# Kernel optimization log

Measured on AMD Instinct MI355X. Metric: run time of the kernel, lower is better.

## Reference

```python
import jax, jax.numpy as jnp
import numpy as np

EPROJS = 512
ODIM = 1024
DLAYERS = 2
DUNITS = 512
EMBED_DIM = 512
JOINT_DIM = 512
BLANK = 0
B, TMAX, LMAX = 4, 256, 63


def setup_inputs() -> dict:
    key = jax.random.key(0)
    ks = jax.random.split(key, 20)
    s = 0.05
    embed = jax.random.normal(ks[0], (ODIM, EMBED_DIM), jnp.float32) * s
    embed = embed.at[BLANK].set(0.0)  # padding_idx=blank
    inp = {
        "hs_pad": jax.random.normal(ks[1], (B, TMAX, EPROJS), jnp.float32),
        "hlens": jnp.full((B,), TMAX, jnp.int32),
        "ys_pad": jax.random.randint(ks[2], (B, LMAX), 0, ODIM, jnp.int64),
        "embed": embed,
        "W_ih0": jax.random.normal(ks[3], (4 * DUNITS, EMBED_DIM), jnp.float32) * s,
        "W_hh0": jax.random.normal(ks[4], (4 * DUNITS, DUNITS), jnp.float32) * s,
        "b_ih0": jax.random.normal(ks[5], (4 * DUNITS,), jnp.float32) * s,
        "b_hh0": jax.random.normal(ks[6], (4 * DUNITS,), jnp.float32) * s,
        "W_ih1": jax.random.normal(ks[7], (4 * DUNITS, DUNITS), jnp.float32) * s,
        "W_hh1": jax.random.normal(ks[8], (4 * DUNITS, DUNITS), jnp.float32) * s,
        "b_ih1": jax.random.normal(ks[9], (4 * DUNITS,), jnp.float32) * s,
        "b_hh1": jax.random.normal(ks[10], (4 * DUNITS,), jnp.float32) * s,
        "W_enc": jax.random.normal(ks[11], (JOINT_DIM, EPROJS), jnp.float32) * s,
        "b_enc": jax.random.normal(ks[12], (JOINT_DIM,), jnp.float32) * s,
        "W_dec": jax.random.normal(ks[13], (JOINT_DIM, DUNITS), jnp.float32) * s,
        "W_out": jax.random.normal(ks[14], (ODIM, JOINT_DIM), jnp.float32) * s,
        "b_out": jax.random.normal(ks[15], (ODIM,), jnp.float32) * s,
    }
    return inp


def _lstm_cell(x, h, c, Wih, Whh, bih, bhh):
    g = x @ Wih.T + bih + h @ Whh.T + bhh  # (B, 4*dunits)
    i, f, gg, o = jnp.split(g, 4, axis=-1)  # torch gate order: i, f, g, o
    c2 = jax.nn.sigmoid(f) * c + jax.nn.sigmoid(i) * jnp.tanh(gg)
    h2 = jax.nn.sigmoid(o) * jnp.tanh(c2)
    return h2, c2


def reference(hs_pad, hlens, ys_pad, embed, W_ih0, W_hh0, b_ih0, b_hh0,
              W_ih1, W_hh1, b_ih1, b_hh1, W_enc, b_enc, W_dec, W_out, b_out):
    Bsz = hs_pad.shape[0]
    # ys_in = [blank] + ys  (dropout is eval-mode identity)
    blank_col = jnp.full((Bsz, 1), BLANK, ys_pad.dtype)
    ys_in = jnp.concatenate([blank_col, ys_pad], axis=1)  # (B, U)
    eys = embed[ys_in]  # (B, U, E)

    def step(carry, ey):
        h0, c0, h1, c1 = carry
        h0, c0 = _lstm_cell(ey, h0, c0, W_ih0, W_hh0, b_ih0, b_hh0)
        h1, c1 = _lstm_cell(h0, h1, c1, W_ih1, W_hh1, b_ih1, b_hh1)
        return (h0, c0, h1, c1), h1

    z0 = jnp.zeros((Bsz, DUNITS), hs_pad.dtype)
    _, h_dec = jax.lax.scan(step, (z0, z0, z0, z0), jnp.swapaxes(eys, 0, 1))
    h_dec = jnp.swapaxes(h_dec, 0, 1)  # (B, U, dunits)

    # joint: tanh(lin_enc(h_enc) + lin_dec(h_dec)) -> lin_out
    henc = hs_pad @ W_enc.T + b_enc          # (B, T, J)
    hdec = h_dec @ W_dec.T                   # (B, U, J)
    z = jnp.tanh(henc[:, :, None, :] + hdec[:, None, :, :])  # (B, T, U, J)
    return z @ W_out.T + b_out               # (B, T, U, odim)
```

## Files before the change

### kernel.cpp

```cpp
#include <hip/hip_runtime.h>
#include <hip/hip_bf16.h>
#include <cstdint>
#include <cstddef>

#define DEVINL __device__ __forceinline__

typedef _Float16 f16x8 __attribute__((ext_vector_type(8)));
typedef _Float16 f16x2 __attribute__((ext_vector_type(2)));
typedef float    f32x4 __attribute__((ext_vector_type(4)));

#define SENT 0xFFFFFFFFFFFFFFFFull


DEVINL float fsigm(float x) {
    float e = __expf(-x);
    return __builtin_amdgcn_rcpf(1.f + e);
}
DEVINL float ftanh(float x) {
    float e = __expf(2.f * x);
    return 1.f - 2.f * __builtin_amdgcn_rcpf(e + 1.f);
}

DEVINL float dot8(f16x8 w, f16x8 x, float acc) {
    f16x2 w0{w[0], w[1]}, w1{w[2], w[3]}, w2{w[4], w[5]}, w3{w[6], w[7]};
    f16x2 x0{x[0], x[1]}, x1{x[2], x[3]}, x2{x[4], x[5]}, x3{x[6], x[7]};
    acc = __builtin_amdgcn_fdot2(w0, x0, acc, false);
    acc = __builtin_amdgcn_fdot2(w1, x1, acc, false);
    acc = __builtin_amdgcn_fdot2(w2, x2, acc, false);
    acc = __builtin_amdgcn_fdot2(w3, x3, acc, false);
    return acc;
}

DEVINL void pollrows(const _Float16* __restrict__ H, int slot, int kp,
                     f16x8 out[4][2]) {
    const uint64_t* base = (const uint64_t*)H + (size_t)slot * 512;
    uint64_t w[16];
    for (;;) {
        bool bad = false;
        #pragma unroll
        for (int b = 0; b < 4; ++b) {
            const uint64_t* rp = base + b * 128 + kp * 2;
            w[b * 4 + 0] = __hip_atomic_load(rp,      __ATOMIC_RELAXED, __HIP_MEMORY_SCOPE_AGENT);
            w[b * 4 + 1] = __hip_atomic_load(rp + 1,  __ATOMIC_RELAXED, __HIP_MEMORY_SCOPE_AGENT);
            w[b * 4 + 2] = __hip_atomic_load(rp + 64, __ATOMIC_RELAXED, __HIP_MEMORY_SCOPE_AGENT);
            w[b * 4 + 3] = __hip_atomic_load(rp + 65, __ATOMIC_RELAXED, __HIP_MEMORY_SCOPE_AGENT);
        }
        #pragma unroll
        for (int i = 0; i < 16; ++i) bad |= (w[i] == SENT);
        if (!bad) break;
        __builtin_amdgcn_s_sleep(1);
    }
    #pragma unroll
    for (int b = 0; b < 4; ++b) {
        union { uint64_t u[2]; f16x8 v; } u0, u1;
        u0.u[0] = w[b * 4 + 0]; u0.u[1] = w[b * 4 + 1];
        u1.u[0] = w[b * 4 + 2]; u1.u[1] = w[b * 4 + 3];
        out[b][0] = u0.v;
        out[b][1] = u1.v;
    }
}

__global__ void k_prep_f16(const float* __restrict__ wih0, const float* __restrict__ whh0,
                           const float* __restrict__ wih1, const float* __restrict__ whh1,
                           const float* __restrict__ wout, _Float16* __restrict__ dst, int total) {
    int stride = gridDim.x * blockDim.x;
    for (int i = blockIdx.x * blockDim.x + threadIdx.x; i < total; i += stride) {
        const float* src; int off;
        if      (i < (1 << 20)) { src = wih0; off = i; }
        else if (i < (2 << 20)) { src = whh0; off = i - (1 << 20); }
        else if (i < (3 << 20)) { src = wih1; off = i - (2 << 20); }
        else if (i < (4 << 20)) { src = whh1; off = i - (3 << 20); }
        else                    { src = wout; off = i - (4 << 20); }
        dst[i] = (_Float16)src[off];
    }
}

__global__ void k_embed(const float* __restrict__ embed, const int* __restrict__ ys,
                        _Float16* __restrict__ Ebuf) {
    int bu = blockIdx.x;
    int b = bu >> 6, u = bu & 63;
    int tok = (u == 0) ? 0 : ys[b * 63 + (u - 1)];
    const float* src = embed + (size_t)tok * 512;
    _Float16* dst = Ebuf + ((size_t)(u * 4 + b)) * 512;
    int t2 = threadIdx.x * 2;
    float2 v = *(const float2*)(src + t2);
    dst[t2]     = (_Float16)v.x;
    dst[t2 + 1] = (_Float16)v.y;
}

DEVINL void gemm_small_body(const float* __restrict__ A, const float* __restrict__ Bt,
                            const float* __restrict__ bias, float* __restrict__ C,
                            int blk) {
    __shared__ float As[64 * 68];
    __shared__ float Bs[64 * 68];
    int bn = blk & 7;
    int bm = blk >> 3;
    int m0 = bm * 64, n0 = bn * 64;
    int tid = threadIdx.x;
    int tx = tid & 15, ty = tid >> 4;
    float acc[4][4] = {};
    for (int k0 = 0; k0 < 512; k0 += 64) {
        __syncthreads();
        #pragma unroll
        for (int i = 0; i < 4; ++i) {
            int fid = i * 256 + tid;
            int rr = fid >> 4, c4 = (fid & 15) * 4;
            *(float4*)(As + rr * 68 + c4) = *(const float4*)(A + (size_t)(m0 + rr) * 512 + k0 + c4);
            *(float4*)(Bs + rr * 68 + c4) = *(const float4*)(Bt + (size_t)(n0 + rr) * 512 + k0 + c4);
        }
        __syncthreads();
        #pragma unroll 4
        for (int kk = 0; kk < 64; kk += 4) {
            float4 a4[4], b4[4];
            #pragma unroll
            for (int ii = 0; ii < 4; ++ii) a4[ii] = *(const float4*)(As + (ty + ii * 16) * 68 + kk);
            #pragma unroll
            for (int jjx = 0; jjx < 4; ++jjx) b4[jjx] = *(const float4*)(Bs + (tx + jjx * 16) * 68 + kk);
            #pragma unroll
            for (int ii = 0; ii < 4; ++ii)
                #pragma unroll
                for (int jjx = 0; jjx < 4; ++jjx)
                    acc[ii][jjx] += a4[ii].x * b4[jjx].x + a4[ii].y * b4[jjx].y +
                                    a4[ii].z * b4[jjx].z + a4[ii].w * b4[jjx].w;
        }
    }
    #pragma unroll
    for (int ii = 0; ii < 4; ++ii) {
        int m = m0 + ty + ii * 16;
        #pragma unroll
        for (int jjx = 0; jjx < 4; ++jjx) {
            int n = n0 + tx + jjx * 16;
            float v = acc[ii][jjx] + (bias ? bias[n] : 0.f);
            C[(size_t)m * 512 + n] = v;
        }
    }
}

__global__ void __launch_bounds__(256) k_gemm_small(
        const float* __restrict__ A, const float* __restrict__ Bt,
        const float* __restrict__ bias, float* __restrict__ C) {
    gemm_small_body(A, Bt, bias, C, blockIdx.x);
}

__global__ void __launch_bounds__(256, 1) k_lstm(
        const _Float16* __restrict__ WF,
        const float* __restrict__ bih0, const float* __restrict__ bhh0,
        const float* __restrict__ bih1, const float* __restrict__ bhh1,
        const _Float16* __restrict__ Ebuf,
        _Float16* __restrict__ H0h, _Float16* __restrict__ H1h,
        float* __restrict__ H1,
        const float* __restrict__ hs, const float* __restrict__ wenc,
        const float* __restrict__ benc, float* __restrict__ henc) {
    if (blockIdx.x >= 64) {
        gemm_small_body(hs, wenc, benc, henc, blockIdx.x - 64);
        return;
    }
    const int blk   = blockIdx.x;
    const int layer = blk >> 5;
    const int ublk  = blk & 31;
    const int unit0 = ublk * 16;
    const int tid   = threadIdx.x;
    const int rg    = tid >> 5;
    const int kp    = tid & 31;

    const int rb_own   = rg * 8 + (kp >> 2);
    const int b_own    = kp & 3;
    const int grow_own = ((rb_own >> 4) << 9) + unit0 + (rb_own & 15);

    const _Float16* WihL = WF + (size_t)(layer ? (2u << 20) : 0u);
    const _Float16* WhhL = WF + (size_t)(layer ? (3u << 20) : (1u << 20));

    f16x8 wA[8][2];
    f16x8 wB[8][2];
    #pragma unroll
    for (int r = 0; r < 8; ++r) {
        int rb = rg * 8 + r;
        int grow = ((rb >> 4) << 9) + unit0 + (rb & 15);
        const _Float16* irow = WihL + (size_t)grow * 512;
        const _Float16* hrow = WhhL + (size_t)grow * 512;
        wA[r][0] = *(const f16x8*)(irow + kp * 8);
        wA[r][1] = *(const f16x8*)(irow + 256 + kp * 8);
        wB[r][0] = *(const f16x8*)(hrow + kp * 8);
        wB[r][1] = *(const f16x8*)(hrow + 256 + kp * 8);
    }
    const float* biL = layer ? bih1 : bih0;
    const float* bhL = layer ? bhh1 : bhh0;
    const float bsum = biL[grow_own] + bhL[grow_own];

    __shared__ float g_lds[64 * 4];

    float c_reg = 0.f;
    const int c0 = kp * 8;
    const int c1 = 256 + kp * 8;
    const int s_lo = layer ? 1 : 0;
    const int s_hi = layer ? 64 : 63;

    for (int s = s_lo; s <= s_hi; ++s) {
        const int st = s - s_lo;

        float p[8][4];
        #pragma unroll
        for (int r = 0; r < 8; ++r)
            #pragma unroll
            for (int b = 0; b < 4; ++b) p[r][b] = 0.f;

        if (!layer) {
            #pragma unroll
            for (int b = 0; b < 4; ++b) {
                const _Float16* er = Ebuf + ((size_t)(st * 4 + b)) * 512;
                f16x8 x0 = *(const f16x8*)(er + c0);
                f16x8 x1 = *(const f16x8*)(er + c1);
                #pragma unroll
                for (int r = 0; r < 8; ++r) {
                    p[r][b] = dot8(wA[r][0], x0, p[r][b]);
                    p[r][b] = dot8(wA[r][1], x1, p[r][b]);
                }
            }
            if (st > 0) {
                f16x8 hv[4][2];
                pollrows(H0h, st - 1, kp, hv);
                #pragma unroll
                for (int b = 0; b < 4; ++b)
                    #pragma unroll
                    for (int r = 0; r < 8; ++r) {
                        p[r][b] = dot8(wB[r][0], hv[b][0], p[r][b]);
                        p[r][b] = dot8(wB[r][1], hv[b][1], p[r][b]);
                    }
            }
        } else {
            f16x8 xv[4][2];
            pollrows(H0h, st, kp, xv);
            #pragma unroll
            for (int b = 0; b < 4; ++b)
                #pragma unroll
                for (int r = 0; r < 8; ++r) {
                    p[r][b] = dot8(wA[r][0], xv[b][0], p[r][b]);
                    p[r][b] = dot8(wA[r][1], xv[b][1], p[r][b]);
                }
            if (st > 0) {
                f16x8 hv[4][2];
                pollrows(H1h, st - 1, kp, hv);
                #pragma unroll
                for (int b = 0; b < 4; ++b)
                    #pragma unroll
                    for (int r = 0; r < 8; ++r) {
                        p[r][b] = dot8(wB[r][0], hv[b][0], p[r][b]);
                        p[r][b] = dot8(wB[r][1], hv[b][1], p[r][b]);
                    }
            }
        }

        float a[32];
        #pragma unroll
        for (int t = 0; t < 32; ++t) a[t] = p[t >> 2][t & 3];
        #pragma unroll
        for (int m = 16; m >= 1; m >>= 1) {
            const bool hi = (kp & m) != 0;
            #pragma unroll
            for (int i = 0; i < m; ++i) {
                float give = hi ? a[i] : a[i + m];
                float got  = __shfl_xor(give, m, 64);
                a[i] = (hi ? a[i + m] : a[i]) + got;
            }
        }
        g_lds[rb_own * 4 + b_own] = a[0] + bsum;
        __syncthreads();

        if (tid < 64) {
            int jj = tid >> 2, b4 = tid & 3;
            float gi = g_lds[(0  + jj) * 4 + b4];
            float gf = g_lds[(16 + jj) * 4 + b4];
            float gg = g_lds[(32 + jj) * 4 + b4];
            float go = g_lds[(48 + jj) * 4 + b4];
            c_reg = fsigm(gf) * c_reg + fsigm(gi) * ftanh(gg);
            float h2 = fsigm(go) * ftanh(c_reg);
            _Float16 h16 = (_Float16)h2;
            unsigned short hb;
            __builtin_memcpy(&hb, &h16, 2);
            int hv0 = (int)hb;
            int hv1 = __shfl_down(hv0, 4, 64);
            int hv2 = __shfl_down(hv0, 8, 64);
            int hv3 = __shfl_down(hv0, 12, 64);
            if ((jj & 3) == 0) {
                uint64_t pk = (uint64_t)(hv0 & 0xFFFF)
                            | ((uint64_t)(hv1 & 0xFFFF) << 16)
                            | ((uint64_t)(hv2 & 0xFFFF) << 32)
                            | ((uint64_t)(hv3 & 0xFFFF) << 48);
                _Float16* dst = (layer ? H1h : H0h) + (size_t)((st << 2) + b4) * 512 + unit0 + jj;
                __hip_atomic_store((uint64_t*)dst, pk,
                                   __ATOMIC_RELAXED, __HIP_MEMORY_SCOPE_AGENT);
            }
            if (layer) {
                int hu = unit0 + jj;
                __hip_atomic_store(H1 + ((size_t)(b4 * 64 + st)) * 512 + hu, h2,
                                   __ATOMIC_RELAXED, __HIP_MEMORY_SCOPE_AGENT);
            }
        }
        __syncthreads();
    }
}

__global__ void __launch_bounds__(512, 1) k_joint(
        const float* __restrict__ henc, const float* __restrict__ hdec,
        const _Float16* __restrict__ Wo, const float* __restrict__ b_out,
        float* __restrict__ out) {
    __shared__ _Float16 As[128 * 512];

    const int d   = blockIdx.x;
    const int bm  = (d & 7) * 64 + (d >> 3);
    const int m0  = bm * 128;
    const int b   = m0 >> 14;
    const int t0  = (m0 & 16383) >> 6;
    const int tid = threadIdx.x;

    {
        const int r  = tid >> 2;
        const int kq = tid & 3;
        const int t  = t0 + (r >> 6);
        const int u  = r & 63;
        const float* he = henc + ((size_t)(b * 256 + t)) * 512 + kq * 128;
        const float* hd = hdec + ((size_t)(b * 64 + u)) * 512 + kq * 128;
        _Float16* dst = As + r * 512;
        const int swz = r & 7;
        #pragma unroll
        for (int i = 0; i < 16; ++i) {
            float4 a  = *(const float4*)(he + i * 8);
            float4 a2 = *(const float4*)(he + i * 8 + 4);
            float4 c  = *(const float4*)(hd + i * 8);
            float4 c2 = *(const float4*)(hd + i * 8 + 4);
            f16x8 z8;
            z8[0] = (_Float16)ftanh(a.x + c.x);
            z8[1] = (_Float16)ftanh(a.y + c.y);
            z8[2] = (_Float16)ftanh(a.z + c.z);
            z8[3] = (_Float16)ftanh(a.w + c.w);
            z8[4] = (_Float16)ftanh(a2.x + c2.x);
            z8[5] = (_Float16)ftanh(a2.y + c2.y);
            z8[6] = (_Float16)ftanh(a2.z + c2.z);
            z8[7] = (_Float16)ftanh(a2.w + c2.w);
            int cs = (kq * 16 + i) ^ swz;
            *(f16x8*)(dst + cs * 8) = z8;
        }
    }
    __syncthreads();

    const int wave = tid >> 6, lane = tid & 63;
    const int l16 = lane & 15, quad = lane >> 4;
    const int wm = wave >> 2;
    const int wn = wave & 3;
    const int swr = l16 & 7;

    for (int nc = 0; nc < 4; ++nc) {
        f32x4 acc[4][4];
        #pragma unroll
        for (int i = 0; i < 4; ++i)
            #pragma unroll
            for (int jx = 0; jx < 4; ++jx) acc[i][jx] = f32x4{0.f, 0.f, 0.f, 0.f};
        const int n_base = nc * 256 + wn * 64;

        #pragma unroll 4
        for (int step = 0; step < 16; ++step) {
            const int k0 = step * 32;
            const int cs = (step * 4 + quad) ^ swr;
            f16x8 af[4], bfv[4];
            #pragma unroll
            for (int i = 0; i < 4; ++i) {
                int row = wm * 64 + i * 16 + l16;
                af[i] = *(const f16x8*)(As + row * 512 + cs * 8);
            }
            #pragma unroll
            for (int jx = 0; jx < 4; ++jx) {
                int n = n_base + jx * 16 + l16;
                bfv[jx] = *(const f16x8*)(Wo + (size_t)n * 512 + k0 + quad * 8);
            }
            #pragma unroll
            for (int i = 0; i < 4; ++i)
                #pragma unroll
                for (int jx = 0; jx < 4; ++jx)
                    acc[i][jx] = __builtin_amdgcn_mfma_f32_16x16x32_f16(af[i], bfv[jx], acc[i][jx], 0, 0, 0);
        }

        #pragma unroll
        for (int i = 0; i < 4; ++i) {
            int mrow = m0 + wm * 64 + i * 16 + quad * 4;
            #pragma unroll
            for (int jx = 0; jx < 4; ++jx) {
                int col = n_base + jx * 16 + l16;
                float bo = b_out[col];
                float* po = out + (size_t)mrow * 1024 + col;
                po[0]    = acc[i][jx][0] + bo;
                po[1024] = acc[i][jx][1] + bo;
                po[2048] = acc[i][jx][2] + bo;
                po[3072] = acc[i][jx][3] + bo;
            }
        }
    }
}

extern "C" void kernel_launch(void* const* d_in, const int* in_sizes, int n_in,
                              void* d_out, int out_size, void* d_ws, size_t ws_size,
                              hipStream_t stream) {
    const float* hs    = (const float*)d_in[0];
    const int*   ys    = (const int*)d_in[2];
    const float* embed = (const float*)d_in[3];
    const float* wih0  = (const float*)d_in[4];
    const float* whh0  = (const float*)d_in[5];
    const float* bih0  = (const float*)d_in[6];
    const float* bhh0  = (const float*)d_in[7];
    const float* wih1  = (const float*)d_in[8];
    const float* whh1  = (const float*)d_in[9];
    const float* bih1  = (const float*)d_in[10];
    const float* bhh1  = (const float*)d_in[11];
    const float* wenc  = (const float*)d_in[12];
    const float* benc  = (const float*)d_in[13];
    const float* wdec  = (const float*)d_in[14];
    const float* wout  = (const float*)d_in[15];
    const float* bout  = (const float*)d_in[16];
    float* out = (float*)d_out;

    char* ws = (char*)d_ws;
    _Float16* WF     = (_Float16*)(ws);
    _Float16* Ebuf16 = (_Float16*)(ws + 9u  * 1024 * 1024);
    _Float16* H0h    = (_Float16*)(ws + 9u  * 1024 * 1024 + 512u * 1024);
    _Float16* H1h    = (_Float16*)(ws + 9u  * 1024 * 1024 + 768u * 1024);
    float* H1    = (float*)(ws + 10u * 1024 * 1024);
    float* henc  = (float*)(ws + 10u * 1024 * 1024 + 512u * 1024);
    float* hdec  = (float*)(ws + 12u * 1024 * 1024 + 512u * 1024);

    hipMemsetAsync(ws + 9u * 1024 * 1024 + 512u * 1024, 0xFF, 512u * 1024, stream);
    k_prep_f16<<<2048, 256, 0, stream>>>(wih0, whh0, wih1, whh1, wout, WF, 4718592);
    k_embed<<<256, 256, 0, stream>>>(embed, ys, Ebuf16);
    k_lstm<<<192, 256, 0, stream>>>(WF, bih0, bhh0, bih1, bhh1, Ebuf16,
                                    H0h, H1h, H1, hs, wenc, benc, henc);
    k_gemm_small<<<32, 256, 0, stream>>>(H1, wdec, nullptr, hdec);
    k_joint<<<512, 512, 0, stream>>>(henc, hdec, WF + (4u << 20), bout, out);
}
```

Measured before the change: 688.8 us.

## Remap LSTM gate rows for in-wave cell update; double-buffer joint GEMM loads

Each wave of the LSTM recurrence kernel now owns the i/f/g/o gate rows of two units. The cell update can therefore be done with wave shuffles instead of an LDS round trip and two block-wide barriers per timestep. Empty asm constraints pin the weight registers. Separately, the joint GEMM inner loop is restructured to software double-buffer A/B fragment loads against MFMA issue, at the cost of more live registers.

```diff
diff --git a/kernel.cpp b/kernel.cpp
--- a/kernel.cpp
+++ b/kernel.cpp
@@ -162,10 +162,7 @@
     const int tid   = threadIdx.x;
     const int rg    = tid >> 5;
     const int kp    = tid & 31;
-
-    const int rb_own   = rg * 8 + (kp >> 2);
-    const int b_own    = kp & 3;
-    const int grow_own = ((rb_own >> 4) << 9) + unit0 + (rb_own & 15);
+    const int lane  = tid & 63;
 
     const _Float16* WihL = WF + (size_t)(layer ? (2u << 20) : 0u);
     const _Float16* WhhL = WF + (size_t)(layer ? (3u << 20) : (1u << 20));
@@ -174,8 +171,8 @@
     f16x8 wB[8][2];
     #pragma unroll
     for (int r = 0; r < 8; ++r) {
-        int rb = rg * 8 + r;
-        int grow = ((rb >> 4) << 9) + unit0 + (rb & 15);
+        int u2 = r >> 2, g = r & 3;
+        int grow = g * 512 + unit0 + rg * 2 + u2;
         const _Float16* irow = WihL + (size_t)grow * 512;
         const _Float16* hrow = WhhL + (size_t)grow * 512;
         wA[r][0] = *(const f16x8*)(irow + kp * 8);
@@ -183,11 +180,23 @@
         wB[r][0] = *(const f16x8*)(hrow + kp * 8);
         wB[r][1] = *(const f16x8*)(hrow + 256 + kp * 8);
     }
+    #pragma unroll
+    for (int r = 0; r < 8; ++r)
+        asm volatile("" : "+v"(wA[r][0]), "+v"(wA[r][1]),
+                          "+v"(wB[r][0]), "+v"(wB[r][1]));
+
+    const int gate_own = (kp >> 2) & 3;
+    const int u2_own   = kp >> 4;
+    const int b_own    = kp & 3;
+    const int ul_own   = rg * 2 + u2_own;
+    const int grow_own = gate_own * 512 + unit0 + ul_own;
+    const bool own     = ((kp & 12) == 0);
+
     const float* biL = layer ? bih1 : bih0;
     const float* bhL = layer ? bhh1 : bhh0;
     const float bsum = biL[grow_own] + bhL[grow_own];
 
-    __shared__ float g_lds[64 * 4];
+    const int w4 = (tid >> 6) * 4;
 
     float c_reg = 0.f;
     const int c0 = kp * 8;
@@ -263,40 +272,34 @@
                 a[i] = (hi ? a[i + m] : a[i]) + got;
             }
         }
-        g_lds[rb_own * 4 + b_own] = a[0] + bsum;
-        __syncthreads();
-
-        if (tid < 64) {
-            int jj = tid >> 2, b4 = tid & 3;
-            float gi = g_lds[(0  + jj) * 4 + b4];
-            float gf = g_lds[(16 + jj) * 4 + b4];
-            float gg = g_lds[(32 + jj) * 4 + b4];
-            float go = g_lds[(48 + jj) * 4 + b4];
-            c_reg = fsigm(gf) * c_reg + fsigm(gi) * ftanh(gg);
-            float h2 = fsigm(go) * ftanh(c_reg);
-            _Float16 h16 = (_Float16)h2;
-            unsigned short hb;
-            __builtin_memcpy(&hb, &h16, 2);
-            int hv0 = (int)hb;
-            int hv1 = __shfl_down(hv0, 4, 64);
-            int hv2 = __shfl_down(hv0, 8, 64);
-            int hv3 = __shfl_down(hv0, 12, 64);
-            if ((jj & 3) == 0) {
-                uint64_t pk = (uint64_t)(hv0 & 0xFFFF)
-                            | ((uint64_t)(hv1 & 0xFFFF) << 16)
-                            | ((uint64_t)(hv2 & 0xFFFF) << 32)
-                            | ((uint64_t)(hv3 & 0xFFFF) << 48);
-                _Float16* dst = (layer ? H1h : H0h) + (size_t)((st << 2) + b4) * 512 + unit0 + jj;
-                __hip_atomic_store((uint64_t*)dst, pk,
-                                   __ATOMIC_RELAXED, __HIP_MEMORY_SCOPE_AGENT);
-            }
-            if (layer) {
-                int hu = unit0 + jj;
-                __hip_atomic_store(H1 + ((size_t)(b4 * 64 + st)) * 512 + hu, h2,
-                                   __ATOMIC_RELAXED, __HIP_MEMORY_SCOPE_AGENT);
-            }
-        }
-        __syncthreads();
+        const float gv = a[0] + bsum;
+
+        float gf = __shfl_down(gv, 4, 64);
+        float gg = __shfl_down(gv, 8, 64);
+        float go = __shfl_down(gv, 12, 64);
+        c_reg = fsigm(gf) * c_reg + fsigm(gv) * ftanh(gg);
+        float h2 = fsigm(go) * ftanh(c_reg);
+
+        _Float16 h16 = (_Float16)h2;
+        unsigned short hb;
+        __builtin_memcpy(&hb, &h16, 2);
+        int hv0 = (int)hb;
+        int hv1 = __shfl_down(hv0, 16, 64);
+        int hv2 = __shfl_down(hv0, 32, 64);
+        int hv3 = __shfl_down(hv0, 48, 64);
+        if (lane < 4) {
+            uint64_t pk = (uint64_t)(hv0 & 0xFFFF)
+                        | ((uint64_t)(hv1 & 0xFFFF) << 16)
+                        | ((uint64_t)(hv2 & 0xFFFF) << 32)
+                        | ((uint64_t)(hv3 & 0xFFFF) << 48);
+            _Float16* dst = (layer ? H1h : H0h) + (size_t)((st << 2) + lane) * 512 + unit0 + w4;
+            __hip_atomic_store((uint64_t*)dst, pk,
+                               __ATOMIC_RELAXED, __HIP_MEMORY_SCOPE_AGENT);
+        }
+        if (layer && own) {
+            __hip_atomic_store(H1 + ((size_t)(b_own * 64 + st)) * 512 + unit0 + ul_own, h2,
+                               __ATOMIC_RELAXED, __HIP_MEMORY_SCOPE_AGENT);
+        }
     }
 }
 
@@ -349,6 +352,30 @@
     const int wn = wave & 3;
     const int swr = l16 & 7;
 
+#define LOADSTEP(S, AF, BF) do {                                             \
+        const int k0_ = (S) * 32;                                            \
+        const int cs_ = ((S) * 4 + quad) ^ swr;                              \
+        _Pragma("unroll")                                                    \
+        for (int i_ = 0; i_ < 4; ++i_) {                                     \
+            int row_ = wm * 64 + i_ * 16 + l16;                              \
+            AF[i_] = *(const f16x8*)(As + row_ * 512 + cs_ * 8);             \
+        }                                                                    \
+        _Pragma("unroll")                                                    \
+        for (int j_ = 0; j_ < 4; ++j_) {                                     \
+            int n_ = n_base + j_ * 16 + l16;                                 \
+            BF[j_] = *(const f16x8*)(Wo + (size_t)n_ * 512 + k0_ + quad * 8);\
+        }                                                                    \
+    } while (0)
+
+#define MFMASTEP(AF, BF) do {                                                \
+        _Pragma("unroll")                                                    \
+        for (int i_ = 0; i_ < 4; ++i_)                                       \
+            _Pragma("unroll")                                                \
+            for (int j_ = 0; j_ < 4; ++j_)                                   \
+                acc[i_][j_] = __builtin_amdgcn_mfma_f32_16x16x32_f16(        \
+                    AF[i_], BF[j_], acc[i_][j_], 0, 0, 0);                   \
+    } while (0)
+
     for (int nc = 0; nc < 4; ++nc) {
         f32x4 acc[4][4];
         #pragma unroll
@@ -357,26 +384,14 @@
             for (int jx = 0; jx < 4; ++jx) acc[i][jx] = f32x4{0.f, 0.f, 0.f, 0.f};
         const int n_base = nc * 256 + wn * 64;
 
-        #pragma unroll 4
-        for (int step = 0; step < 16; ++step) {
-            const int k0 = step * 32;
-            const int cs = (step * 4 + quad) ^ swr;
-            f16x8 af[4], bfv[4];
-            #pragma unroll
-            for (int i = 0; i < 4; ++i) {
-                int row = wm * 64 + i * 16 + l16;
-                af[i] = *(const f16x8*)(As + row * 512 + cs * 8);
-            }
-            #pragma unroll
-            for (int jx = 0; jx < 4; ++jx) {
-                int n = n_base + jx * 16 + l16;
-                bfv[jx] = *(const f16x8*)(Wo + (size_t)n * 512 + k0 + quad * 8);
-            }
-            #pragma unroll
-            for (int i = 0; i < 4; ++i)
-                #pragma unroll
-                for (int jx = 0; jx < 4; ++jx)
-                    acc[i][jx] = __builtin_amdgcn_mfma_f32_16x16x32_f16(af[i], bfv[jx], acc[i][jx], 0, 0, 0);
+        f16x8 afA[4], bfA[4], afB[4], bfB[4];
+        LOADSTEP(0, afA, bfA);
+        #pragma unroll
+        for (int step = 0; step < 16; step += 2) {
+            if (step + 1 < 16) LOADSTEP(step + 1, afB, bfB);
+            MFMASTEP(afA, bfA);
+            if (step + 2 < 16) LOADSTEP(step + 2, afA, bfA);
+            MFMASTEP(afB, bfB);
         }
 
         #pragma unroll
@@ -394,6 +409,8 @@
             }
         }
     }
+#undef LOADSTEP
+#undef MFMASTEP
 }
 
 extern "C" void kernel_launch(void* const* d_in, const int* in_sizes, int n_in,
```

New measurement: 1.594 ms. 131% more time.
